# Kernel tuning notes

Measured on AMD Instinct MI355X. Metric: run time of the kernel, lower is better.

## Reference

```python
import jax, jax.numpy as jnp
import numpy as np

B, S, H, T, F, L = 32, 512, 1024, 100, 512, 5  # batch, seq, hidden, num_topics, topic_hidden, n_langs
EPS = 1e-5


def _layernorm(x, g, b):
    mu = jnp.mean(x, axis=-1, keepdims=True)
    var = jnp.mean((x - mu) ** 2, axis=-1, keepdims=True)
    return (x - mu) * jax.lax.rsqrt(var + EPS) * g + b


def setup_inputs() -> dict:
    key = jax.random.key(0)
    ks = jax.random.split(key, 16)
    sc = 0.02
    return {
        "sequence_output": jax.random.normal(ks[0], (B, S, H), dtype=jnp.float32),
        "attention_mask": jnp.ones((B, S), dtype=jnp.float32),
        "language_ids": jax.random.randint(ks[1], (B,), 0, L, dtype=jnp.int32),
        "lda_features": jax.random.uniform(ks[2], (B, T), dtype=jnp.float32),
        # per-language adapter params (stacked over L)
        "W1": jax.random.normal(ks[3], (L, H, H), dtype=jnp.float32) * sc,
        "b1": jnp.zeros((L, H), dtype=jnp.float32),
        "g1": jnp.ones((L, H), dtype=jnp.float32),
        "beta1": jnp.zeros((L, H), dtype=jnp.float32),
        "W2": jax.random.normal(ks[4], (L, H, H), dtype=jnp.float32) * sc,
        "b2": jnp.zeros((L, H), dtype=jnp.float32),
        # topic fusion params
        "Wf": jax.random.normal(ks[5], (H + T, F), dtype=jnp.float32) * sc,
        "bf": jnp.zeros((F,), dtype=jnp.float32),
        "gf": jnp.ones((F,), dtype=jnp.float32),
        "betaf": jnp.zeros((F,), dtype=jnp.float32),
    }


def reference(sequence_output, attention_mask, language_ids, lda_features,
              W1, b1, g1, beta1, W2, b2, Wf, bf, gf, betaf):
    # Apply every language adapter to the full batch, then mask-accumulate
    # (faithful to the original anti-pattern).
    adapted = jnp.zeros_like(sequence_output)
    for lang in range(L):
        h = jnp.einsum("bsh,he->bse", sequence_output, W1[lang]) + b1[lang]
        h = jax.nn.relu(_layernorm(h, g1[lang], beta1[lang]))
        h = jnp.einsum("bsh,he->bse", h, W2[lang]) + b2[lang]
        lang_mask = (language_ids == lang).astype(sequence_output.dtype)[:, None, None]
        adapted = adapted + lang_mask * h
    # masked mean pool over sequence
    masked = adapted * attention_mask[:, :, None]
    pooled = masked.sum(axis=1) / attention_mask.sum(axis=1)[:, None]  # [B, H]
    combined = jnp.concatenate([pooled, lda_features], axis=-1)        # [B, H+T]
    fused = _layernorm(combined @ Wf + bf, gf, betaf)
    return jax.nn.relu(fused)  # dropout is identity in eval
```

## Files before the change

### kernel.cpp

```cpp
#include <hip/hip_runtime.h>
#include <hip/hip_bf16.h>
#include <stdint.h>

#define Bq 32
#define Sq 512
#define Hq 1024
#define Tq 100
#define Fq 512
#define Lq 5
#define EPSq 1e-5f

typedef float fx4 __attribute__((ext_vector_type(4)));
typedef __bf16 bfx8 __attribute__((ext_vector_type(8)));
typedef unsigned short u16x8 __attribute__((ext_vector_type(8)));

static __device__ __forceinline__ unsigned short f2bf(float f) {
  unsigned int u = __builtin_bit_cast(unsigned int, f);
  return (unsigned short)((u + 0x7fffu + ((u >> 16) & 1u)) >> 16);
}
static __device__ __forceinline__ float bf2f(unsigned short s) {
  return __builtin_bit_cast(float, ((unsigned int)s) << 16);
}
static __device__ __forceinline__ u16x8 cvt8(float4 x0, float4 x1) {
  u16x8 r;
  r[0] = f2bf(x0.x); r[1] = f2bf(x0.y); r[2] = f2bf(x0.z); r[3] = f2bf(x0.w);
  r[4] = f2bf(x1.x); r[5] = f2bf(x1.y); r[6] = f2bf(x1.z); r[7] = f2bf(x1.w);
  return r;
}
static __device__ __forceinline__ void gl_lds16(const void* g, void* l) {
  __builtin_amdgcn_global_load_lds(
      (const __attribute__((address_space(1))) unsigned int*)(uintptr_t)g,
      (__attribute__((address_space(3))) unsigned int*)(uintptr_t)l,
      16, 0, 0);
}

__global__ void k_prep(const float* __restrict__ w1, unsigned short* __restrict__ w1t) {
  __shared__ float t[32][33];
  int blk = blockIdx.x;
  int l = blk >> 10; int rem = blk & 1023; int tr = rem >> 5; int tc = rem & 31;
  const float* src = w1 + (size_t)l * Hq * Hq;
  unsigned short* dst = w1t + (size_t)l * Hq * Hq;
  int tid = threadIdx.x;
  int tx = tid & 31, ty = tid >> 5;
#pragma unroll
  for (int p = 0; p < 4; p++)
    t[ty + 8 * p][tx] = src[(size_t)(tr * 32 + ty + 8 * p) * Hq + tc * 32 + tx];
  __syncthreads();
#pragma unroll
  for (int p = 0; p < 4; p++)
    dst[(size_t)(tc * 32 + ty + 8 * p) * Hq + tr * 32 + tx] = f2bf(t[tx][ty + 8 * p]);
}

__global__ __launch_bounds__(512, 2) void k_gemm1(const float* __restrict__ seq,
                                                  const unsigned short* __restrict__ w1t,
                                                  const float* __restrict__ b1,
                                                  const int* __restrict__ lid,
                                                  unsigned short* __restrict__ h1bf) {
  __shared__ short sA[4][256 * 32];
  __shared__ short sB[4][256 * 32];
  int bid = blockIdx.x;
  int g = bid & 63; int tn = bid >> 6;
  int b = g >> 1; int tm = g & 1;
  int lang = lid[b];
  const float* Abf = seq + (size_t)b * Sq * Hq + (size_t)tm * 256 * Hq;
  const unsigned short* Bb = w1t + (size_t)lang * Hq * Hq + (size_t)tn * 256 * Hq;

  int tid = threadIdx.x;
  int lane = tid & 63; int wid = tid >> 6;
  int wr = wid >> 2, wc = wid & 3;
  int fr = lane & 15;
  int q = lane >> 4;
  int key = ((fr >> 1) & 7) << 4;

  const float* gAf0; const float* gAf1; int aW0, aW1;
  {
    int c0 = tid;        int R0 = c0 >> 2, q0 = c0 & 3; int y0 = R0 * 64 + q0 * 16;
    int c1 = tid + 512;  int R1 = c1 >> 2, q1 = c1 & 3; int y1 = R1 * 64 + q1 * 16;
    aW0 = y0 ^ ((y0 >> 3) & 0x70);
    aW1 = y1 ^ ((y1 >> 3) & 0x70);
    gAf0 = Abf + (size_t)R0 * Hq + q0 * 8;
    gAf1 = Abf + (size_t)R1 * Hq + q1 * 8;
  }
  const unsigned short* gB[2]; int dstOff[2];
#pragma unroll
  for (int j = 0; j < 2; j++) {
    int p = (tid + j * 512) * 16;
    int l = p ^ ((p >> 3) & 0x70);
    int R = l >> 6, qa = (l >> 4) & 3;
    gB[j] = Bb + (size_t)R * Hq + qa * 8;
    dstOff[j] = p;
  }

  int aOff[8], bOff[4];
#pragma unroll
  for (int m = 0; m < 8; m++)
    aOff[m] = ((wr * 128 + m * 16 + fr) * 64 + q * 16) ^ key;
#pragma unroll
  for (int n = 0; n < 4; n++)
    bOff[n] = ((wc * 64 + n * 16 + fr) * 64 + q * 16) ^ key;

  fx4 acc[8][4];
#pragma unroll
  for (int m = 0; m < 8; m++)
#pragma unroll
    for (int n = 0; n < 4; n++) acc[m][n] = (fx4){0.f, 0.f, 0.f, 0.f};

  float4 ra0a, ra0b, ra1a, ra1b;

#pragma unroll
  for (int t = 0; t < 2; t++) {
    ra0a = *(const float4*)(gAf0 + t * 32); ra0b = *(const float4*)(gAf0 + t * 32 + 4);
    ra1a = *(const float4*)(gAf1 + t * 32); ra1b = *(const float4*)(gAf1 + t * 32 + 4);
    *(u16x8*)((char*)sA[t] + aW0) = cvt8(ra0a, ra0b);
    *(u16x8*)((char*)sA[t] + aW1) = cvt8(ra1a, ra1b);
  }
  ra0a = *(const float4*)(gAf0 + 64); ra0b = *(const float4*)(gAf0 + 68);
  ra1a = *(const float4*)(gAf1 + 64); ra1b = *(const float4*)(gAf1 + 68);
#pragma unroll
  for (int s = 0; s < 3; s++) {
    gl_lds16(gB[0] + s * 32, (char*)sB[s] + dstOff[0]);
    gl_lds16(gB[1] + s * 32, (char*)sB[s] + dstOff[1]);
  }

  for (int hs = 0; hs < 32; hs++) {
    int cur = hs & 3;
    if (hs < 31)
      asm volatile("s_waitcnt vmcnt(4) lgkmcnt(0)\n\ts_barrier" ::: "memory");
    else
      asm volatile("s_waitcnt vmcnt(0) lgkmcnt(0)\n\ts_barrier" ::: "memory");
    if (hs <= 29) {
      int sa = (hs + 2) & 3;
      *(u16x8*)((char*)sA[sa] + aW0) = cvt8(ra0a, ra0b);
      *(u16x8*)((char*)sA[sa] + aW1) = cvt8(ra1a, ra1b);
    }
    if (hs <= 28) {
      int ko = (hs + 3) * 32;
      ra0a = *(const float4*)(gAf0 + ko); ra0b = *(const float4*)(gAf0 + ko + 4);
      ra1a = *(const float4*)(gAf1 + ko); ra1b = *(const float4*)(gAf1 + ko + 4);
    }
    if (hs <= 28) {
      int ko = (hs + 3) * 32;
      gl_lds16(gB[0] + ko, (char*)sB[(hs + 3) & 3] + dstOff[0]);
      gl_lds16(gB[1] + ko, (char*)sB[(hs + 3) & 3] + dstOff[1]);
    }
    const char* cA = (const char*)sA[cur];
    const char* cB = (const char*)sB[cur];
    bfx8 bf[4], af[8];
#pragma unroll
    for (int n = 0; n < 4; n++) bf[n] = *(const bfx8*)(cB + bOff[n]);
#pragma unroll
    for (int m = 0; m < 8; m++) af[m] = *(const bfx8*)(cA + aOff[m]);
    __builtin_amdgcn_s_setprio(1);
#pragma unroll
    for (int m = 0; m < 8; m++)
#pragma unroll
      for (int n = 0; n < 4; n++)
        acc[m][n] = __builtin_amdgcn_mfma_f32_16x16x32_bf16(af[m], bf[n], acc[m][n], 0, 0, 0);
    __builtin_amdgcn_s_setprio(0);
  }

  unsigned short* Cb = h1bf + (size_t)b * Sq * Hq;
  float bv[4];
#pragma unroll
  for (int n = 0; n < 4; n++)
    bv[n] = b1[lang * Hq + tn * 256 + wc * 64 + n * 16 + fr];
  int r0 = q * 4;
#pragma unroll
  for (int m = 0; m < 8; m++) {
#pragma unroll
    for (int n = 0; n < 4; n++) {
      int col = tn * 256 + wc * 64 + n * 16 + fr;
#pragma unroll
      for (int r = 0; r < 4; r++) {
        int row = tm * 256 + wr * 128 + m * 16 + r0 + r;
        Cb[(size_t)row * Hq + col] = f2bf(acc[m][n][r] + bv[n]);
      }
    }
  }
}

__global__ __launch_bounds__(256) void k_ln_pool(const unsigned short* __restrict__ h1bf,
                                                 const float* __restrict__ g1,
                                                 const float* __restrict__ be1,
                                                 const float* __restrict__ mask,
                                                 const int* __restrict__ lid,
                                                 float* __restrict__ partial) {
  __shared__ float sacc[4][1024];
  int blk = blockIdx.x; int b = blk >> 3; int ch = blk & 7;
  int tid = threadIdx.x; int lane = tid & 63; int w = tid >> 6;
  int lang = lid[b];
  int e0 = lane * 8;
  int e1 = 512 + lane * 8;

  const float4* gp = (const float4*)(g1 + (size_t)lang * Hq);
  const float4* bp = (const float4*)(be1 + (size_t)lang * Hq);
  float4 ga0 = gp[lane * 2], ga1 = gp[lane * 2 + 1];
  float4 gb0 = gp[128 + lane * 2], gb1 = gp[129 + lane * 2];
  float4 ba0 = bp[lane * 2], ba1 = bp[lane * 2 + 1];
  float4 bb0 = bp[128 + lane * 2], bb1 = bp[129 + lane * 2];
  float gA[8] = {ga0.x, ga0.y, ga0.z, ga0.w, ga1.x, ga1.y, ga1.z, ga1.w};
  float gB[8] = {gb0.x, gb0.y, gb0.z, gb0.w, gb1.x, gb1.y, gb1.z, gb1.w};
  float bA[8] = {ba0.x, ba0.y, ba0.z, ba0.w, ba1.x, ba1.y, ba1.z, ba1.w};
  float bB[8] = {bb0.x, bb0.y, bb0.z, bb0.w, bb1.x, bb1.y, bb1.z, bb1.w};

  float acc0[8] = {0, 0, 0, 0, 0, 0, 0, 0}, acc1[8] = {0, 0, 0, 0, 0, 0, 0, 0};

  for (int i = 0; i < 16; i++) {
    int s = ch * 64 + w * 16 + i;
    const unsigned short* rowp = h1bf + ((size_t)b * Sq + s) * Hq;
    u16x8 va = *(const u16x8*)(rowp + e0);
    u16x8 vb = *(const u16x8*)(rowp + e1);
    float xa[8], xb[8];
    float sum = 0.f, sq = 0.f;
#pragma unroll
    for (int j = 0; j < 8; j++) {
      xa[j] = bf2f(va[j]); sum += xa[j]; sq += xa[j] * xa[j];
      xb[j] = bf2f(vb[j]); sum += xb[j]; sq += xb[j] * xb[j];
    }
#pragma unroll
    for (int off = 1; off < 64; off <<= 1) {
      sum += __shfl_xor(sum, off, 64);
      sq += __shfl_xor(sq, off, 64);
    }
    float mu = sum * (1.f / Hq);
    float var = sq * (1.f / Hq) - mu * mu;
    float rstd = rsqrtf(var + EPSq);
    float mw = mask[b * Sq + s];
#pragma unroll
    for (int j = 0; j < 8; j++) {
      float y0 = fmaxf((xa[j] - mu) * rstd * gA[j] + bA[j], 0.f);
      float y1 = fmaxf((xb[j] - mu) * rstd * gB[j] + bB[j], 0.f);
      acc0[j] += mw * y0;
      acc1[j] += mw * y1;
    }
  }
#pragma unroll
  for (int j = 0; j < 8; j++) {
    sacc[w][e0 + j] = acc0[j];
    sacc[w][e1 + j] = acc1[j];
  }
  __syncthreads();
  int e = tid * 4;
#pragma unroll
  for (int j = 0; j < 4; j++)
    partial[(size_t)blk * Hq + e + j] =
        sacc[0][e + j] + sacc[1][e + j] + sacc[2][e + j] + sacc[3][e + j];
}

__global__ __launch_bounds__(256) void k_gemm2p(const float* __restrict__ partial,
                                                const float* __restrict__ mask,
                                                const float* __restrict__ w2,
                                                const int* __restrict__ lid,
                                                float* __restrict__ g2part) {
  __shared__ float pl[256];
  __shared__ float wsum[4];
  int blk = blockIdx.x;
  int b = blk >> 3; int ch = (blk >> 2) & 1; int ks = blk & 3;
  int tid = threadIdx.x;
  int lang = lid[b];
  float mv = mask[b * Sq + tid] + mask[b * Sq + 256 + tid];
#pragma unroll
  for (int off = 1; off < 64; off <<= 1) mv += __shfl_xor(mv, off, 64);
  if ((tid & 63) == 0) wsum[tid >> 6] = mv;
  __syncthreads();
  float inv = 1.0f / (wsum[0] + wsum[1] + wsum[2] + wsum[3]);
  float s = 0.f;
#pragma unroll
  for (int c = 0; c < 8; c++) s += partial[((size_t)(b * 8 + c)) * Hq + ks * 256 + tid];
  pl[tid] = s * inv;
  __syncthreads();
  int col = ch * 512 + tid * 2;
  const float* W = w2 + (size_t)lang * Hq * Hq + (size_t)ks * 256 * Hq + col;
  float a0 = 0.f, a1 = 0.f;
  for (int e0 = 0; e0 < 256; e0 += 8) {
    float2 w[8];
#pragma unroll
    for (int j = 0; j < 8; j++) w[j] = *(const float2*)(W + (size_t)(e0 + j) * Hq);
#pragma unroll
    for (int j = 0; j < 8; j++) { float c = pl[e0 + j]; a0 += c * w[j].x; a1 += c * w[j].y; }
  }
  float2* dst = (float2*)(g2part + ((size_t)(b * 4 + ks) * Hq) + col);
  *dst = make_float2(a0, a1);
}

__global__ __launch_bounds__(256) void k_fpart(const float* __restrict__ g2part,
                                               const float* __restrict__ b2,
                                               const int* __restrict__ lid,
                                               const float* __restrict__ lda,
                                               const float* __restrict__ wf,
                                               float* __restrict__ fpart) {
  __shared__ float sc[128];
  int blk = blockIdx.x;
  int b = blk / 9, ks = blk % 9;
  int tid = threadIdx.x;
  int klen = (ks < 8) ? 128 : 100;
  int kbase = (ks < 8) ? ks * 128 : Hq;
  if (ks < 8) {
    if (tid < 128) {
      int col = kbase + tid;
      float v = b2[lid[b] * Hq + col];
#pragma unroll
      for (int c = 0; c < 4; c++) v += g2part[((size_t)(b * 4 + c)) * Hq + col];
      sc[tid] = v;
    }
  } else if (tid < 100) {
    sc[tid] = lda[b * Tq + tid];
  }
  __syncthreads();
  const float* W = wf + (size_t)kbase * Fq + tid * 2;
  float a0 = 0.f, a1 = 0.f;
  int k0 = 0;
  for (; k0 + 8 <= klen; k0 += 8) {
    float2 w[8];
#pragma unroll
    for (int j = 0; j < 8; j++) w[j] = *(const float2*)(W + (size_t)(k0 + j) * Fq);
#pragma unroll
    for (int j = 0; j < 8; j++) { float c = sc[k0 + j]; a0 += c * w[j].x; a1 += c * w[j].y; }
  }
  for (; k0 < klen; k0++) {
    float2 w = *(const float2*)(W + (size_t)k0 * Fq);
    float c = sc[k0];
    a0 += c * w.x; a1 += c * w.y;
  }
  float2* dst = (float2*)(fpart + (size_t)blk * Fq + tid * 2);
  *dst = make_float2(a0, a1);
}

__global__ __launch_bounds__(512) void k_final2(const float* __restrict__ fpart,
                                                const float* __restrict__ bff,
                                                const float* __restrict__ gf,
                                                const float* __restrict__ betaf,
                                                float* __restrict__ out) {
  __shared__ float rsum[8], rsq[8];
  int b = blockIdx.x; int tid = threadIdx.x;
  float acc = bff[tid];
#pragma unroll
  for (int ks = 0; ks < 9; ks++) acc += fpart[((size_t)b * 9 + ks) * Fq + tid];
  float s = acc, q = acc * acc;
#pragma unroll
  for (int off = 1; off < 64; off <<= 1) {
    s += __shfl_xor(s, off, 64);
    q += __shfl_xor(q, off, 64);
  }
  int w = tid >> 6, lane = tid & 63;
  if (lane == 0) { rsum[w] = s; rsq[w] = q; }
  __syncthreads();
  float S = 0.f, Q = 0.f;
#pragma unroll
  for (int i = 0; i < 8; i++) { S += rsum[i]; Q += rsq[i]; }
  float mu = S * (1.f / Fq);
  float var = Q * (1.f / Fq) - mu * mu;
  float y = (acc - mu) * rsqrtf(var + EPSq) * gf[tid] + betaf[tid];
  y = fmaxf(y, 0.f);
  out[b * Fq + tid] = y;
}

extern "C" void kernel_launch(void* const* d_in, const int* in_sizes, int n_in,
                              void* d_out, int out_size, void* d_ws, size_t ws_size,
                              hipStream_t stream) {
  const float* seq = (const float*)d_in[0];
  const float* mask = (const float*)d_in[1];
  const int* lid = (const int*)d_in[2];
  const float* lda = (const float*)d_in[3];
  const float* W1 = (const float*)d_in[4];
  const float* b1 = (const float*)d_in[5];
  const float* g1 = (const float*)d_in[6];
  const float* be1 = (const float*)d_in[7];
  const float* W2 = (const float*)d_in[8];
  const float* b2 = (const float*)d_in[9];
  const float* Wf = (const float*)d_in[10];
  const float* bff = (const float*)d_in[11];
  const float* gf = (const float*)d_in[12];
  const float* betaf = (const float*)d_in[13];
  float* out = (float*)d_out;

  char* ws = (char*)d_ws;
  unsigned short* w1t = (unsigned short*)(ws);
  unsigned short* h1bf = (unsigned short*)(ws + 10485760);
  float* partial = (float*)(ws + 44040192);
  float* g2part = (float*)(ws + 45088768);
  float* fpart = (float*)(ws + 45613056);

  k_prep<<<5120, 256, 0, stream>>>(W1, w1t);
  k_gemm1<<<256, 512, 0, stream>>>(seq, w1t, b1, lid, h1bf);
  k_ln_pool<<<256, 256, 0, stream>>>(h1bf, g1, be1, mask, lid, partial);
  k_gemm2p<<<256, 256, 0, stream>>>(partial, mask, W2, lid, g2part);
  k_fpart<<<288, 256, 0, stream>>>(g2part, b2, lid, lda, Wf, fpart);
  k_final2<<<32, 512, 0, stream>>>(fpart, bff, gf, betaf, out);
}
```

Baseline: 91.23 us.

## Reorder GEMM1 pipeline: issue loads first, defer A-tile convert/store after MFMAs

Restructures the k_gemm1 main loop into a two-way unrolled macro with ping-pong register sets for the fp32 A prefetch. Global loads for the next stages are issued before the MFMA block, and the bf16 conversion and LDS store of the A tile is moved after the MFMAs, with sched_barriers pinning the order and a deeper vmcnt wait. The goal is to hide the conversion and LDS-write latency behind the matrix math. It also swaps the manual rounding for the library bf16 conversion. The extra live float4 registers could raise register pressure at two waves per SIMD.

```diff
diff --git a/kernel.cpp b/kernel.cpp
--- a/kernel.cpp
+++ b/kernel.cpp
@@ -21,10 +21,14 @@
 static __device__ __forceinline__ float bf2f(unsigned short s) {
   return __builtin_bit_cast(float, ((unsigned int)s) << 16);
 }
+static __device__ __forceinline__ unsigned short bfbits(float f) {
+  __hip_bfloat16 h = __float2bfloat16(f);
+  return __builtin_bit_cast(unsigned short, h);
+}
 static __device__ __forceinline__ u16x8 cvt8(float4 x0, float4 x1) {
   u16x8 r;
-  r[0] = f2bf(x0.x); r[1] = f2bf(x0.y); r[2] = f2bf(x0.z); r[3] = f2bf(x0.w);
-  r[4] = f2bf(x1.x); r[5] = f2bf(x1.y); r[6] = f2bf(x1.z); r[7] = f2bf(x1.w);
+  r[0] = bfbits(x0.x); r[1] = bfbits(x0.y); r[2] = bfbits(x0.z); r[3] = bfbits(x0.w);
+  r[4] = bfbits(x1.x); r[5] = bfbits(x1.y); r[6] = bfbits(x1.z); r[7] = bfbits(x1.w);
   return r;
 }
 static __device__ __forceinline__ void gl_lds16(const void* g, void* l) {
@@ -50,6 +54,45 @@
   for (int p = 0; p < 4; p++)
     dst[(size_t)(tc * 32 + ty + 8 * p) * Hq + tr * 32 + tx] = f2bf(t[tx][ty + 8 * p]);
 }
+
+#define HS_ITER(HS, C0A, C0B, C1A, C1B, N0A, N0B, N1A, N1B)                          \
+  do {                                                                               \
+    int cur = (HS) & 3;                                                              \
+    if ((HS) < 30)                                                                   \
+      asm volatile("s_waitcnt vmcnt(6) lgkmcnt(0)\n\ts_barrier" ::: "memory");       \
+    else if ((HS) == 30)                                                             \
+      asm volatile("s_waitcnt vmcnt(2) lgkmcnt(0)\n\ts_barrier" ::: "memory");       \
+    else                                                                             \
+      asm volatile("s_waitcnt vmcnt(0) lgkmcnt(0)\n\ts_barrier" ::: "memory");       \
+    if ((HS) <= 28) {                                                                \
+      int ko = ((HS) + 3) * 32;                                                      \
+      N0A = *(const float4*)(gAf0 + ko); N0B = *(const float4*)(gAf0 + ko + 4);      \
+      N1A = *(const float4*)(gAf1 + ko); N1B = *(const float4*)(gAf1 + ko + 4);      \
+      int slot = ((HS) + 3) & 3;                                                     \
+      gl_lds16(gB[0] + ko, (char*)sB[slot] + dstOff[0]);                             \
+      gl_lds16(gB[1] + ko, (char*)sB[slot] + dstOff[1]);                             \
+    }                                                                                \
+    __builtin_amdgcn_sched_barrier(0);                                               \
+    const char* cA = (const char*)sA[cur];                                           \
+    const char* cB = (const char*)sB[cur];                                           \
+    bfx8 bfr[4], af[8];                                                              \
+    _Pragma("unroll") for (int n = 0; n < 4; n++)                                    \
+        bfr[n] = *(const bfx8*)(cB + bOff[n]);                                       \
+    _Pragma("unroll") for (int m = 0; m < 8; m++)                                    \
+        af[m] = *(const bfx8*)(cA + aOff[m]);                                        \
+    __builtin_amdgcn_s_setprio(1);                                                   \
+    _Pragma("unroll") for (int m = 0; m < 8; m++)                                    \
+      _Pragma("unroll") for (int n = 0; n < 4; n++)                                  \
+          acc[m][n] = __builtin_amdgcn_mfma_f32_16x16x32_bf16(af[m], bfr[n],         \
+                                                              acc[m][n], 0, 0, 0);  \
+    __builtin_amdgcn_s_setprio(0);                                                   \
+    __builtin_amdgcn_sched_barrier(0);                                               \
+    if ((HS) <= 29) {                                                                \
+      int sa = ((HS) + 2) & 3;                                                       \
+      *(u16x8*)((char*)sA[sa] + aW0) = cvt8(C0A, C0B);                               \
+      *(u16x8*)((char*)sA[sa] + aW1) = cvt8(C1A, C1B);                               \
+    }                                                                                \
+  } while (0)
 
 __global__ __launch_bounds__(512, 2) void k_gemm1(const float* __restrict__ seq,
                                                   const unsigned short* __restrict__ w1t,
@@ -74,8 +117,8 @@
 
   const float* gAf0; const float* gAf1; int aW0, aW1;
   {
-    int c0 = tid;        int R0 = c0 >> 2, q0 = c0 & 3; int y0 = R0 * 64 + q0 * 16;
-    int c1 = tid + 512;  int R1 = c1 >> 2, q1 = c1 & 3; int y1 = R1 * 64 + q1 * 16;
+    int c0 = tid;       int R0 = c0 >> 2, q0 = c0 & 3; int y0 = R0 * 64 + q0 * 16;
+    int c1 = tid + 512; int R1 = c1 >> 2, q1 = c1 & 3; int y1 = R1 * 64 + q1 * 16;
     aW0 = y0 ^ ((y0 >> 3) & 0x70);
     aW1 = y1 ^ ((y1 >> 3) & 0x70);
     gAf0 = Abf + (size_t)R0 * Hq + q0 * 8;
@@ -105,58 +148,29 @@
 #pragma unroll
     for (int n = 0; n < 4; n++) acc[m][n] = (fx4){0.f, 0.f, 0.f, 0.f};
 
-  float4 ra0a, ra0b, ra1a, ra1b;
-
-#pragma unroll
-  for (int t = 0; t < 2; t++) {
-    ra0a = *(const float4*)(gAf0 + t * 32); ra0b = *(const float4*)(gAf0 + t * 32 + 4);
-    ra1a = *(const float4*)(gAf1 + t * 32); ra1b = *(const float4*)(gAf1 + t * 32 + 4);
-    *(u16x8*)((char*)sA[t] + aW0) = cvt8(ra0a, ra0b);
-    *(u16x8*)((char*)sA[t] + aW1) = cvt8(ra1a, ra1b);
-  }
-  ra0a = *(const float4*)(gAf0 + 64); ra0b = *(const float4*)(gAf0 + 68);
-  ra1a = *(const float4*)(gAf1 + 64); ra1b = *(const float4*)(gAf1 + 68);
-#pragma unroll
-  for (int s = 0; s < 3; s++) {
-    gl_lds16(gB[0] + s * 32, (char*)sB[s] + dstOff[0]);
-    gl_lds16(gB[1] + s * 32, (char*)sB[s] + dstOff[1]);
-  }
-
-  for (int hs = 0; hs < 32; hs++) {
-    int cur = hs & 3;
-    if (hs < 31)
-      asm volatile("s_waitcnt vmcnt(4) lgkmcnt(0)\n\ts_barrier" ::: "memory");
-    else
-      asm volatile("s_waitcnt vmcnt(0) lgkmcnt(0)\n\ts_barrier" ::: "memory");
-    if (hs <= 29) {
-      int sa = (hs + 2) & 3;
-      *(u16x8*)((char*)sA[sa] + aW0) = cvt8(ra0a, ra0b);
-      *(u16x8*)((char*)sA[sa] + aW1) = cvt8(ra1a, ra1b);
-    }
-    if (hs <= 28) {
-      int ko = (hs + 3) * 32;
-      ra0a = *(const float4*)(gAf0 + ko); ra0b = *(const float4*)(gAf0 + ko + 4);
-      ra1a = *(const float4*)(gAf1 + ko); ra1b = *(const float4*)(gAf1 + ko + 4);
-    }
-    if (hs <= 28) {
-      int ko = (hs + 3) * 32;
-      gl_lds16(gB[0] + ko, (char*)sB[(hs + 3) & 3] + dstOff[0]);
-      gl_lds16(gB[1] + ko, (char*)sB[(hs + 3) & 3] + dstOff[1]);
-    }
-    const char* cA = (const char*)sA[cur];
-    const char* cB = (const char*)sB[cur];
-    bfx8 bf[4], af[8];
-#pragma unroll
-    for (int n = 0; n < 4; n++) bf[n] = *(const bfx8*)(cB + bOff[n]);
-#pragma unroll
-    for (int m = 0; m < 8; m++) af[m] = *(const bfx8*)(cA + aOff[m]);
-    __builtin_amdgcn_s_setprio(1);
-#pragma unroll
-    for (int m = 0; m < 8; m++)
-#pragma unroll
-      for (int n = 0; n < 4; n++)
-        acc[m][n] = __builtin_amdgcn_mfma_f32_16x16x32_bf16(af[m], bf[n], acc[m][n], 0, 0, 0);
-    __builtin_amdgcn_s_setprio(0);
+  {
+    float4 t0a = *(const float4*)(gAf0);      float4 t0b = *(const float4*)(gAf0 + 4);
+    float4 t1a = *(const float4*)(gAf1);      float4 t1b = *(const float4*)(gAf1 + 4);
+    *(u16x8*)((char*)sA[0] + aW0) = cvt8(t0a, t0b);
+    *(u16x8*)((char*)sA[0] + aW1) = cvt8(t1a, t1b);
+    t0a = *(const float4*)(gAf0 + 32); t0b = *(const float4*)(gAf0 + 36);
+    t1a = *(const float4*)(gAf1 + 32); t1b = *(const float4*)(gAf1 + 36);
+    *(u16x8*)((char*)sA[1] + aW0) = cvt8(t0a, t0b);
+    *(u16x8*)((char*)sA[1] + aW1) = cvt8(t1a, t1b);
+  }
+  gl_lds16(gB[0],      (char*)sB[0] + dstOff[0]);
+  gl_lds16(gB[1],      (char*)sB[0] + dstOff[1]);
+  gl_lds16(gB[0] + 32, (char*)sB[1] + dstOff[0]);
+  gl_lds16(gB[1] + 32, (char*)sB[1] + dstOff[1]);
+  float4 rc0a, rc0b, rc1a, rc1b, rn0a, rn0b, rn1a, rn1b;
+  rc0a = *(const float4*)(gAf0 + 64); rc0b = *(const float4*)(gAf0 + 68);
+  rc1a = *(const float4*)(gAf1 + 64); rc1b = *(const float4*)(gAf1 + 68);
+  gl_lds16(gB[0] + 64, (char*)sB[2] + dstOff[0]);
+  gl_lds16(gB[1] + 64, (char*)sB[2] + dstOff[1]);
+
+  for (int hs = 0; hs < 32; hs += 2) {
+    HS_ITER(hs,     rc0a, rc0b, rc1a, rc1b, rn0a, rn0b, rn1a, rn1b);
+    HS_ITER(hs + 1, rn0a, rn0b, rn1a, rn1b, rc0a, rc0b, rc1a, rc1b);
   }
 
   unsigned short* Cb = h1bf + (size_t)b * Sq * Hq;
```

Measured after the change: 92.96 us. About the same (+1.9%).
